# Optimization experiments

Measured on AMD Instinct MI355X. Metric: run time of the kernel, lower is better.

## Reference

```python
import jax, jax.numpy as jnp
import numpy as np

MASK_VAL = float(-2**32 + 1)


def setup_inputs() -> dict:
    key = jax.random.key(0)
    k1, k2, k3, k4 = jax.random.split(key, 4)
    B, L, D = 16, 1024, 512
    user_embedding = jax.random.normal(k1, (B, L, D), dtype=jnp.float32)
    hyper_embedding = jax.random.normal(k2, (B, L, D), dtype=jnp.float32)
    # xavier_normal for Linear(2D -> D): std = sqrt(2 / (fan_in + fan_out))
    std = float(np.sqrt(2.0 / (2 * D + D)))
    W1 = jax.random.normal(k3, (D, 2 * D), dtype=jnp.float32) * std
    W2 = jax.random.normal(k4, (D, 2 * D), dtype=jnp.float32) * std
    b1 = jnp.zeros((D,), dtype=jnp.float32)
    b2 = jnp.zeros((D,), dtype=jnp.float32)
    return {"user_embedding": user_embedding, "hyper_embedding": hyper_embedding,
            "W1": W1, "b1": b1, "W2": W2, "b2": b2}


def reference(user_embedding, hyper_embedding, W1, b1, W2, b2):
    B, L, D = user_embedding.shape
    index = jnp.concatenate([user_embedding, hyper_embedding], axis=-1)  # [B,L,2D]
    Q = jnp.einsum('blk,dk->bld', index, W1) + b1  # [B,L,D]
    K = jnp.einsum('blk,dk->bld', index, W2) + b2  # [B,L,D]
    # torch: Q_K = einsum('bld,bmd->bml', Q, K) -> Q_K[b,m,l] = <Q[b,l], K[b,m]>
    Q_K = jnp.einsum('bld,bmd->bml', Q, K) / (D ** 0.5 + 1e-6)
    # upper-triangular (incl. diagonal) additive mask of -2^32+1
    mask = jnp.triu(jnp.full((L, L), MASK_VAL, dtype=Q_K.dtype))
    score = jax.nn.softmax(Q_K + mask, axis=-1)  # [B,L,L]
    # torch: output = einsum('bll,bmd->bld', score, user_embedding)
    #  -> diag(score)[b,l] * sum_m user_embedding[b,m,d]
    diag = jnp.diagonal(score, axis1=1, axis2=2)  # [B,L]
    summed = jnp.sum(user_embedding, axis=1, keepdims=True)  # [B,1,D]
    return diag[..., None] * summed  # [B,L,D]
```

## Files before the change

kernel.cpp:

```cpp
#include <hip/hip_runtime.h>


namespace {

constexpr int B  = 16;
constexpr int L  = 1024;
constexpr int D  = 512;
constexpr int MG  = 64;
constexpr int MPG = L / MG;
constexpr int TPB = D / 4;

__global__ void partial_sum_kernel(const float* __restrict__ user,
                                   float* __restrict__ partial) {
    const int blk = blockIdx.x;
    const int b   = blk >> 6;
    const int g   = blk & (MG - 1);
    const int d4  = threadIdx.x;
    const float4* src = reinterpret_cast<const float4*>(
        user + (size_t)(b * L + g * MPG) * D) + d4;
    float4 acc = make_float4(0.f, 0.f, 0.f, 0.f);
#pragma unroll
    for (int m = 0; m < MPG; ++m) {
        float4 v = src[(size_t)m * (D / 4)];
        acc.x += v.x; acc.y += v.y; acc.z += v.z; acc.w += v.w;
    }
    reinterpret_cast<float4*>(partial + (size_t)(b * MG + g) * D)[d4] = acc;
}

__global__ void fill_row0_kernel(const float* __restrict__ partial,
                                 float* __restrict__ out) {
    const int b  = blockIdx.x;
    const int d4 = threadIdx.x;
    const float4* p = reinterpret_cast<const float4*>(
        partial + (size_t)b * MG * D) + d4;
    float4 acc = make_float4(0.f, 0.f, 0.f, 0.f);
#pragma unroll 8
    for (int g = 0; g < MG; ++g) {
        float4 v = p[(size_t)g * (D / 4)];
        acc.x += v.x; acc.y += v.y; acc.z += v.z; acc.w += v.w;
    }
    const float s = 1.0f / 1024.0f;
    acc.x *= s; acc.y *= s; acc.z *= s; acc.w *= s;
    reinterpret_cast<float4*>(out + (size_t)b * L * D)[d4] = acc;
}

__global__ void direct_row0_kernel(const float* __restrict__ user,
                                   float* __restrict__ out) {
    const int b  = blockIdx.x;
    const int d4 = threadIdx.x;
    const float4* src = reinterpret_cast<const float4*>(
        user + (size_t)b * L * D) + d4;
    float4 acc = make_float4(0.f, 0.f, 0.f, 0.f);
    for (int m = 0; m < L; ++m) {
        float4 v = src[(size_t)m * (D / 4)];
        acc.x += v.x; acc.y += v.y; acc.z += v.z; acc.w += v.w;
    }
    const float s = 1.0f / 1024.0f;
    acc.x *= s; acc.y *= s; acc.z *= s; acc.w *= s;
    reinterpret_cast<float4*>(out + (size_t)b * L * D)[d4] = acc;
}

}

extern "C" void kernel_launch(void* const* d_in, const int* in_sizes, int n_in,
                              void* d_out, int out_size, void* d_ws, size_t ws_size,
                              hipStream_t stream) {
    const float* user = (const float*)d_in[0];
    float* out = (float*)d_out;

    hipMemsetAsync(d_out, 0, (size_t)out_size * sizeof(float), stream);

    const size_t partial_bytes = (size_t)B * MG * D * sizeof(float);
    if (ws_size >= partial_bytes) {
        float* partial = (float*)d_ws;
        partial_sum_kernel<<<B * MG, TPB, 0, stream>>>(user, partial);
        fill_row0_kernel<<<B, TPB, 0, stream>>>(partial, out);
    } else {
        direct_row0_kernel<<<B, TPB, 0, stream>>>(user, out);
    }
}
```

Measured before the change: 22.26 us.

## Fuse output zeroing into partial-sum kernel and parallelize final reduction

Drops the separate memset of the 32MB output. The partial-sum kernel now writes zeros to the output rows it reads, in the same pass. Partition count doubles to 128 groups of 8 rows. The final reduce kernel uses 512 threads that split the partials four ways and combine them through shared memory. This saves one launch and overlaps the zero stores with the input reads, but the fill kernel must still run after all zeroing, which the stream order guarantees.

```diff
diff --git a/kernel.cpp b/kernel.cpp
--- a/kernel.cpp
+++ b/kernel.cpp
@@ -3,45 +3,61 @@
 
 namespace {
 
-constexpr int B  = 16;
-constexpr int L  = 1024;
-constexpr int D  = 512;
-constexpr int MG  = 64;
+constexpr int B   = 16;
+constexpr int L   = 1024;
+constexpr int D   = 512;
+constexpr int MG  = 128;
 constexpr int MPG = L / MG;
 constexpr int TPB = D / 4;
 
-__global__ void partial_sum_kernel(const float* __restrict__ user,
-                                   float* __restrict__ partial) {
+__global__ void fused_zero_partial_kernel(const float* __restrict__ user,
+                                          float* __restrict__ out,
+                                          float* __restrict__ partial) {
     const int blk = blockIdx.x;
-    const int b   = blk >> 6;
+    const int b   = blk >> 7;
     const int g   = blk & (MG - 1);
     const int d4  = threadIdx.x;
-    const float4* src = reinterpret_cast<const float4*>(
-        user + (size_t)(b * L + g * MPG) * D) + d4;
-    float4 acc = make_float4(0.f, 0.f, 0.f, 0.f);
+    const size_t base = (size_t)(b * L + g * MPG) * D;
+    const float4* src = reinterpret_cast<const float4*>(user + base) + d4;
+    float4*       dst = reinterpret_cast<float4*>(out + base) + d4;
+    const float4 z = make_float4(0.f, 0.f, 0.f, 0.f);
+    float4 acc = z;
 #pragma unroll
     for (int m = 0; m < MPG; ++m) {
         float4 v = src[(size_t)m * (D / 4)];
         acc.x += v.x; acc.y += v.y; acc.z += v.z; acc.w += v.w;
+        dst[(size_t)m * (D / 4)] = z;
     }
     reinterpret_cast<float4*>(partial + (size_t)(b * MG + g) * D)[d4] = acc;
 }
 
 __global__ void fill_row0_kernel(const float* __restrict__ partial,
                                  float* __restrict__ out) {
-    const int b  = blockIdx.x;
-    const int d4 = threadIdx.x;
+    const int b    = blockIdx.x;
+    const int d4   = threadIdx.x & (TPB - 1);
+    const int part = threadIdx.x >> 7;
     const float4* p = reinterpret_cast<const float4*>(
-        partial + (size_t)b * MG * D) + d4;
+        partial + (size_t)(b * MG + part * (MG / 4)) * D) + d4;
     float4 acc = make_float4(0.f, 0.f, 0.f, 0.f);
 #pragma unroll 8
-    for (int g = 0; g < MG; ++g) {
+    for (int g = 0; g < MG / 4; ++g) {
         float4 v = p[(size_t)g * (D / 4)];
         acc.x += v.x; acc.y += v.y; acc.z += v.z; acc.w += v.w;
     }
-    const float s = 1.0f / 1024.0f;
-    acc.x *= s; acc.y *= s; acc.z *= s; acc.w *= s;
-    reinterpret_cast<float4*>(out + (size_t)b * L * D)[d4] = acc;
+    __shared__ float4 sdata[4][TPB];
+    sdata[part][d4] = acc;
+    __syncthreads();
+    if (part == 0) {
+        float4 a0 = sdata[0][d4], a1 = sdata[1][d4];
+        float4 a2 = sdata[2][d4], a3 = sdata[3][d4];
+        const float s = 1.0f / 1024.0f;
+        float4 r;
+        r.x = (a0.x + a1.x + a2.x + a3.x) * s;
+        r.y = (a0.y + a1.y + a2.y + a3.y) * s;
+        r.z = (a0.z + a1.z + a2.z + a3.z) * s;
+        r.w = (a0.w + a1.w + a2.w + a3.w) * s;
+        reinterpret_cast<float4*>(out + (size_t)b * L * D)[d4] = r;
+    }
 }
 
 __global__ void direct_row0_kernel(const float* __restrict__ user,
@@ -68,14 +84,13 @@
     const float* user = (const float*)d_in[0];
     float* out = (float*)d_out;
 
-    hipMemsetAsync(d_out, 0, (size_t)out_size * sizeof(float), stream);
-
     const size_t partial_bytes = (size_t)B * MG * D * sizeof(float);
     if (ws_size >= partial_bytes) {
         float* partial = (float*)d_ws;
-        partial_sum_kernel<<<B * MG, TPB, 0, stream>>>(user, partial);
-        fill_row0_kernel<<<B, TPB, 0, stream>>>(partial, out);
+        fused_zero_partial_kernel<<<B * MG, TPB, 0, stream>>>(user, out, partial);
+        fill_row0_kernel<<<B, 4 * TPB, 0, stream>>>(partial, out);
     } else {
+        hipMemsetAsync(d_out, 0, (size_t)out_size * sizeof(float), stream);
         direct_row0_kernel<<<B, TPB, 0, stream>>>(user, out);
     }
 }
```

After: 19.12 us. 1.16x faster.

## Fuse output zeroing into finalize kernel and halve partial-sum groups

Applied to the files above, without the earlier changes.

Drops the separate hipMemsetAsync over the whole output. Zeroing now happens inside the finalize kernel with nontemporal stores, spread over B*64 blocks, one of which per batch also reduces the partials for row 0 using two thread halves and shared memory. The partial-sum stage uses 32 groups instead of 64 and nontemporal loads. This removes one launch and the memset pass, in exchange for more logic in the finalize kernel and fewer partial-sum blocks.

```diff
diff --git a/kernel.cpp b/kernel.cpp
--- a/kernel.cpp
+++ b/kernel.cpp
@@ -3,61 +3,86 @@
 
 namespace {
 
-constexpr int B  = 16;
-constexpr int L  = 1024;
-constexpr int D  = 512;
-constexpr int MG  = 64;
-constexpr int MPG = L / MG;
-constexpr int TPB = D / 4;
+typedef float f32x4 __attribute__((ext_vector_type(4)));
+
+constexpr int B    = 16;
+constexpr int L    = 1024;
+constexpr int D    = 512;
+constexpr int MG   = 32;
+constexpr int MPG  = L / MG;
+constexpr int TPBA = D / 4;
 
 __global__ void partial_sum_kernel(const float* __restrict__ user,
                                    float* __restrict__ partial) {
     const int blk = blockIdx.x;
-    const int b   = blk >> 6;
+    const int b   = blk >> 5;
     const int g   = blk & (MG - 1);
     const int d4  = threadIdx.x;
-    const float4* src = reinterpret_cast<const float4*>(
+    const f32x4* src = reinterpret_cast<const f32x4*>(
         user + (size_t)(b * L + g * MPG) * D) + d4;
-    float4 acc = make_float4(0.f, 0.f, 0.f, 0.f);
-#pragma unroll
+    f32x4 acc = (f32x4)(0.f);
+#pragma unroll 8
     for (int m = 0; m < MPG; ++m) {
-        float4 v = src[(size_t)m * (D / 4)];
-        acc.x += v.x; acc.y += v.y; acc.z += v.z; acc.w += v.w;
+        f32x4 v = __builtin_nontemporal_load(src + (size_t)m * (D / 4));
+        acc += v;
     }
-    reinterpret_cast<float4*>(partial + (size_t)(b * MG + g) * D)[d4] = acc;
+    reinterpret_cast<f32x4*>(partial + (size_t)(b * MG + g) * D)[d4] = acc;
 }
 
-__global__ void fill_row0_kernel(const float* __restrict__ partial,
-                                 float* __restrict__ out) {
-    const int b  = blockIdx.x;
-    const int d4 = threadIdx.x;
-    const float4* p = reinterpret_cast<const float4*>(
-        partial + (size_t)b * MG * D) + d4;
-    float4 acc = make_float4(0.f, 0.f, 0.f, 0.f);
-#pragma unroll 8
-    for (int g = 0; g < MG; ++g) {
-        float4 v = p[(size_t)g * (D / 4)];
-        acc.x += v.x; acc.y += v.y; acc.z += v.z; acc.w += v.w;
+__global__ void zero_and_finalize_kernel(const float* __restrict__ partial,
+                                         float* __restrict__ out) {
+    const int tid = threadIdx.x;
+    const int bid = blockIdx.x;
+    const int b   = bid >> 6;
+    const int r   = bid & 63;
+    f32x4* dst = reinterpret_cast<f32x4*>(out + (size_t)(b * L + r * 16) * D);
+    const f32x4 z = (f32x4)(0.f);
+
+    if (r != 0) {
+#pragma unroll
+        for (int it = 0; it < 8; ++it)
+            __builtin_nontemporal_store(z, dst + it * 256 + tid);
+        return;
     }
-    const float s = 1.0f / 1024.0f;
-    acc.x *= s; acc.y *= s; acc.z *= s; acc.w *= s;
-    reinterpret_cast<float4*>(out + (size_t)b * L * D)[d4] = acc;
+
+#pragma unroll
+    for (int it = 0; it < 8; ++it) {
+        const int idx = it * 256 + tid;
+        if (idx >= D / 4)
+            __builtin_nontemporal_store(z, dst + idx);
+    }
+
+    const int d4   = tid & (TPBA - 1);
+    const int part = tid >> 7;
+    const f32x4* p = reinterpret_cast<const f32x4*>(
+        partial + (size_t)(b * MG + part * (MG / 2)) * D) + d4;
+    f32x4 acc = z;
+#pragma unroll
+    for (int g = 0; g < MG / 2; ++g)
+        acc += p[(size_t)g * (D / 4)];
+    __shared__ f32x4 sdata[2][TPBA];
+    sdata[part][d4] = acc;
+    __syncthreads();
+    if (part == 0) {
+        f32x4 a0 = sdata[0][d4], a1 = sdata[1][d4];
+        const float s = 1.0f / 1024.0f;
+        f32x4 rres = (a0 + a1) * s;
+        dst[d4] = rres;
+    }
 }
 
 __global__ void direct_row0_kernel(const float* __restrict__ user,
                                    float* __restrict__ out) {
     const int b  = blockIdx.x;
     const int d4 = threadIdx.x;
-    const float4* src = reinterpret_cast<const float4*>(
+    const f32x4* src = reinterpret_cast<const f32x4*>(
         user + (size_t)b * L * D) + d4;
-    float4 acc = make_float4(0.f, 0.f, 0.f, 0.f);
-    for (int m = 0; m < L; ++m) {
-        float4 v = src[(size_t)m * (D / 4)];
-        acc.x += v.x; acc.y += v.y; acc.z += v.z; acc.w += v.w;
-    }
+    f32x4 acc = (f32x4)(0.f);
+    for (int m = 0; m < L; ++m)
+        acc += src[(size_t)m * (D / 4)];
     const float s = 1.0f / 1024.0f;
-    acc.x *= s; acc.y *= s; acc.z *= s; acc.w *= s;
-    reinterpret_cast<float4*>(out + (size_t)b * L * D)[d4] = acc;
+    acc *= s;
+    reinterpret_cast<f32x4*>(out + (size_t)b * L * D)[d4] = acc;
 }
 
 }
@@ -68,14 +93,13 @@
     const float* user = (const float*)d_in[0];
     float* out = (float*)d_out;
 
-    hipMemsetAsync(d_out, 0, (size_t)out_size * sizeof(float), stream);
-
     const size_t partial_bytes = (size_t)B * MG * D * sizeof(float);
     if (ws_size >= partial_bytes) {
         float* partial = (float*)d_ws;
-        partial_sum_kernel<<<B * MG, TPB, 0, stream>>>(user, partial);
-        fill_row0_kernel<<<B, TPB, 0, stream>>>(partial, out);
+        partial_sum_kernel<<<B * MG, TPBA, 0, stream>>>(user, partial);
+        zero_and_finalize_kernel<<<B * 64, 256, 0, stream>>>(partial, out);
     } else {
-        direct_row0_kernel<<<B, TPB, 0, stream>>>(user, out);
+        (void)hipMemsetAsync(d_out, 0, (size_t)out_size * sizeof(float), stream);
+        direct_row0_kernel<<<B, TPBA, 0, stream>>>(user, out);
     }
 }
```

Result: faster. 18.79 us (-15.6%).
